# Performance work log

Hardware: AMD Instinct MI355X
Metric: run time of the kernel (lower is better)

Reference implementation:

```python
import jax, jax.numpy as jnp
import numpy as np

N_NODES = 100000
N_EDGES = 1600000
D_FEAT = 64
COS_EPS = 1e-8  # torch.nn.functional.cosine_similarity default eps


def setup_inputs() -> dict:
    key = jax.random.key(0)
    k1, k2 = jax.random.split(key)
    features = jax.random.normal(k1, (N_NODES, D_FEAT), dtype=jnp.float32)
    edge_index = jax.random.randint(k2, (2, N_EDGES), 0, N_NODES, dtype=jnp.int64)
    return {"features": features, "edge_index": edge_index}


def _mean_agg(h, src, dst, n_nodes):
    # copy_u: message = h[src]; fn.mean: per-dst mean over incoming messages
    msg_sum = jax.ops.segment_sum(h[src], dst, num_segments=n_nodes)  # [N, d]
    deg = jax.ops.segment_sum(jnp.ones(src.shape, h.dtype), dst, num_segments=n_nodes)  # [N]
    deg = deg[:, None]
    # nodes with zero in-degree get 0 (DGL mean semantics)
    return jnp.where(deg > 0, msg_sum / jnp.maximum(deg, 1.0), 0.0)


def reference(features, edge_index):
    src, dst = edge_index[0], edge_index[1]
    n = features.shape[0]
    x1 = _mean_agg(features, src, dst, n)   # gcn1
    x2 = _mean_agg(x1, src, dst, n)         # gcn2
    # cosine similarity along feature dim
    dot = jnp.sum(x1 * x2, axis=-1)
    n1 = jnp.linalg.norm(x1, axis=-1)
    n2 = jnp.linalg.norm(x2, axis=-1)
    cos = dot / jnp.maximum(n1 * n2, COS_EPS)
    w = cos[:, None]
    return w * x2 + (1.0 - w) * x1
```

## Files before the change

kernel.cpp:

```cpp
#include <hip/hip_runtime.h>
#include <hip/hip_fp16.h>
#include <math.h>

#define N_NODES 100000
#define N_EDGES 1600000
#define D_FEAT  64

#define NPB     256
#define NBC     ((N_NODES + NPB - 1) / NPB)
#define F1_WGS  512
#define NV4     (N_EDGES / 4)
#define CHUNK_V ((NV4 + F1_WGS - 1) / F1_WGS)
#define RAW_CAP 5120
#define CASTN   ((N_NODES * D_FEAT) / 4)
#define CAST_BLOCKS ((CASTN + 255) / 256)

#define GCAP    68


__device__ __forceinline__ uint4 pack8(const float* v) {
    __half2 h0 = __floats2half2_rn(v[0], v[1]);
    __half2 h1 = __floats2half2_rn(v[2], v[3]);
    __half2 h2 = __floats2half2_rn(v[4], v[5]);
    __half2 h3 = __floats2half2_rn(v[6], v[7]);
    uint4 st;
    st.x = *(unsigned*)&h0; st.y = *(unsigned*)&h1;
    st.z = *(unsigned*)&h2; st.w = *(unsigned*)&h3;
    return st;
}

__device__ __forceinline__ void unp8(uint4 u, float* a) {
    { __half2 h = *(__half2*)&u.x; float2 f = __half22float2(h); a[0]=f.x; a[1]=f.y; }
    { __half2 h = *(__half2*)&u.y; float2 f = __half22float2(h); a[2]=f.x; a[3]=f.y; }
    { __half2 h = *(__half2*)&u.z; float2 f = __half22float2(h); a[4]=f.x; a[5]=f.y; }
    { __half2 h = *(__half2*)&u.w; float2 f = __half22float2(h); a[6]=f.x; a[7]=f.y; }
}

__device__ __forceinline__ void acc4(uint4 u, __half2& h0, __half2& h1,
                                     __half2& h2, __half2& h3) {
    h0 = __hadd2(h0, *(__half2*)&u.x);
    h1 = __hadd2(h1, *(__half2*)&u.y);
    h2 = __hadd2(h2, *(__half2*)&u.z);
    h3 = __hadd2(h3, *(__half2*)&u.w);
}

__device__ __forceinline__ int block_excl_scan_512(int v, int t, int* wsum) {
    int lane = t & 63, wv = t >> 6;
    int incl = v;
    #pragma unroll
    for (int m = 1; m < 64; m <<= 1) {
        int o = __shfl_up(incl, m);
        if (lane >= m) incl += o;
    }
    if (lane == 63) wsum[wv] = incl;
    __syncthreads();
    int prefix = 0;
    #pragma unroll
    for (int j = 0; j < 8; j++)
        if (j < wv) prefix += wsum[j];
    return prefix + incl - v;
}


__global__ void cast_and_hist(const float* __restrict__ feat,
                              __half* __restrict__ feat_h,
                              const int4* __restrict__ dst4,
                              int* __restrict__ percnt) {
    if (blockIdx.x >= F1_WGS) {
        int i = (blockIdx.x - F1_WGS) * 256 + threadIdx.x;
        if (i < CASTN) {
            float4 v = ((const float4*)feat)[i];
            __half2 h0 = __floats2half2_rn(v.x, v.y);
            __half2 h1 = __floats2half2_rn(v.z, v.w);
            uint2 st;
            st.x = *(unsigned*)&h0;
            st.y = *(unsigned*)&h1;
            ((uint2*)feat_h)[i] = st;
        }
        return;
    }
    __shared__ int cnt[NBC];
    for (int i = threadIdx.x; i < NBC; i += blockDim.x) cnt[i] = 0;
    __syncthreads();
    int i0 = blockIdx.x * CHUNK_V;
    int i1 = min(i0 + CHUNK_V, NV4);
    for (int i = i0 + threadIdx.x; i < i1; i += blockDim.x) {
        int4 d = dst4[i];
        atomicAdd(&cnt[d.x >> 8], 1);
        atomicAdd(&cnt[d.y >> 8], 1);
        atomicAdd(&cnt[d.z >> 8], 1);
        atomicAdd(&cnt[d.w >> 8], 1);
    }
    __syncthreads();
    for (int i = threadIdx.x; i < NBC; i += blockDim.x)
        percnt[i * F1_WGS + blockIdx.x] = cnt[i];
}


__global__ __launch_bounds__(F1_WGS) void bucket_colscan(
        int* __restrict__ percnt, int* __restrict__ bhist) {
    __shared__ int wsum[8];
    int b = blockIdx.x, t = threadIdx.x;
    int v = percnt[b * F1_WGS + t];
    int excl = block_excl_scan_512(v, t, wsum);
    percnt[b * F1_WGS + t] = excl;
    if (t == F1_WGS - 1) bhist[b] = excl + v;
}

__global__ __launch_bounds__(512) void bucket_scan(
        const int* __restrict__ bhist, int* __restrict__ bbase) {
    __shared__ int wsum[8];
    int t = threadIdx.x;
    int v = (t < NBC) ? bhist[t] : 0;
    int excl = block_excl_scan_512(v, t, wsum);
    if (t < NBC) bbase[t] = excl;
    if (t == NBC - 1) bbase[NBC] = excl + v;
}

__global__ __launch_bounds__(F1_WGS) void bucketize(
        const int4* __restrict__ src4,
        const int4* __restrict__ dst4,
        const int* __restrict__ bbase,
        const int* __restrict__ percnt,
        unsigned int* __restrict__ tmp1) {
    __shared__ int base[NBC];
    __shared__ int cur[NBC];
    int wg = blockIdx.x, t = threadIdx.x;
    if (t < NBC) {
        base[t] = bbase[t] + percnt[t * F1_WGS + wg];
        cur[t] = 0;
    }
    __syncthreads();
    int i0 = wg * CHUNK_V;
    int i1 = min(i0 + CHUNK_V, NV4);
    for (int i = i0 + t; i < i1; i += F1_WGS) {
        int4 d = dst4[i];
        int4 s = src4[i];
        {
            int b = d.x >> 8; int r = atomicAdd(&cur[b], 1);
            tmp1[base[b] + r] = ((unsigned)s.x << 8) | (unsigned)(d.x & 255);
        }
        {
            int b = d.y >> 8; int r = atomicAdd(&cur[b], 1);
            tmp1[base[b] + r] = ((unsigned)s.y << 8) | (unsigned)(d.y & 255);
        }
        {
            int b = d.z >> 8; int r = atomicAdd(&cur[b], 1);
            tmp1[base[b] + r] = ((unsigned)s.z << 8) | (unsigned)(d.z & 255);
        }
        {
            int b = d.w >> 8; int r = atomicAdd(&cur[b], 1);
            tmp1[base[b] + r] = ((unsigned)s.w << 8) | (unsigned)(d.w & 255);
        }
    }
}

__global__ __launch_bounds__(512) void bucket_csr(
        const unsigned int* __restrict__ tmp1,
        const int* __restrict__ bbase,
        int* __restrict__ offsets,
        int* __restrict__ csr_src) {
    __shared__ int cnt[NPB];
    __shared__ int off[NPB];
    __shared__ int wsum[8];
    __shared__ int buf[RAW_CAP];
    int b = blockIdx.x, t = threadIdx.x;
    int ebase = bbase[b];
    int ecnt  = bbase[b + 1] - ebase;
    int node0 = b * NPB;

    if (t < NPB) cnt[t] = 0;
    __syncthreads();

    if (ecnt <= RAW_CAP) {
        unsigned myv[10];
        #pragma unroll
        for (int k = 0; k < 10; k++) {
            int i = t + k * 512;
            if (i < ecnt) {
                unsigned u = tmp1[ebase + i];
                myv[k] = u;
                atomicAdd(&cnt[u & 255], 1);
            }
        }
        __syncthreads();

        int v = (t < NPB) ? cnt[t] : 0;
        int excl = block_excl_scan_512(v, t, wsum);
        if (t < NPB) {
            off[t] = excl;
            cnt[t] = 0;
            if (node0 + t < N_NODES) offsets[node0 + t] = ebase + excl;
        }
        if (b == NBC - 1 && t == 0) offsets[N_NODES] = N_EDGES;
        __syncthreads();

        #pragma unroll
        for (int k = 0; k < 10; k++) {
            int i = t + k * 512;
            if (i < ecnt) {
                unsigned u = myv[k];
                int d = (int)(u & 255);
                int r = atomicAdd(&cnt[d], 1);
                buf[off[d] + r] = (int)(u >> 8);
            }
        }
        __syncthreads();
        for (int i = t; i < ecnt; i += 512)
            csr_src[ebase + i] = buf[i];
    } else {
        for (int i = t; i < ecnt; i += 512)
            atomicAdd(&cnt[tmp1[ebase + i] & 255], 1);
        __syncthreads();

        int v = (t < NPB) ? cnt[t] : 0;
        int excl = block_excl_scan_512(v, t, wsum);
        if (t < NPB) {
            off[t] = excl;
            cnt[t] = 0;
            if (node0 + t < N_NODES) offsets[node0 + t] = ebase + excl;
        }
        if (b == NBC - 1 && t == 0) offsets[N_NODES] = N_EDGES;
        __syncthreads();

        for (int i = t; i < ecnt; i += 512) {
            unsigned u = tmp1[ebase + i];
            int d = (int)(u & 255);
            int r = atomicAdd(&cnt[d], 1);
            csr_src[ebase + off[d] + r] = (int)(u >> 8);
        }
    }
}


__global__ __launch_bounds__(256) void gather1_kernel(
        const __half* __restrict__ feat_h,
        const int* __restrict__ offsets,
        const int* __restrict__ csr,
        __half* __restrict__ x1_h) {
    __shared__ int snbr[4][8][GCAP];
    int wv   = threadIdx.x >> 6;
    int lane = threadIdx.x & 63;
    int g    = lane >> 3;
    int fl   = lane & 7;
    int node = (blockIdx.x * 4 + wv) * 8 + g;

    int base = offsets[node];
    int deg  = offsets[node + 1] - base;
    int dcap = min(deg, GCAP);

    int* my = snbr[wv][g];
    for (int j = fl; j < dcap; j += 8)
        my[j] = csr[base + j];
    __builtin_amdgcn_wave_barrier();

    __half2 a0 = __float2half2_rn(0.f), a1 = a0, a2 = a0, a3 = a0;
    __half2 b0 = a0, b1 = a0, b2 = a0, b3 = a0;
    const __half* fb = feat_h + (fl << 3);
    int j = 0;
    for (; j + 4 <= dcap; j += 4) {
        int4 s = *(const int4*)&my[j];
        uint4 u0 = *(const uint4*)(fb + ((size_t)s.x << 6));
        uint4 u1 = *(const uint4*)(fb + ((size_t)s.y << 6));
        uint4 u2 = *(const uint4*)(fb + ((size_t)s.z << 6));
        uint4 u3 = *(const uint4*)(fb + ((size_t)s.w << 6));
        acc4(u0, a0, a1, a2, a3);
        acc4(u1, b0, b1, b2, b3);
        acc4(u2, a0, a1, a2, a3);
        acc4(u3, b0, b1, b2, b3);
    }
    for (; j < dcap; ++j) {
        int s = my[j];
        uint4 u = *(const uint4*)(fb + ((size_t)s << 6));
        acc4(u, a0, a1, a2, a3);
    }
    for (j = GCAP; j < deg; ++j) {
        int s = csr[base + j];
        uint4 u = *(const uint4*)(fb + ((size_t)s << 6));
        acc4(u, a0, a1, a2, a3);
    }
    a0 = __hadd2(a0, b0); a1 = __hadd2(a1, b1);
    a2 = __hadd2(a2, b2); a3 = __hadd2(a3, b3);

    float invf = (deg > 0) ? __builtin_amdgcn_rcpf((float)deg) : 0.0f;
    float r[8];
    { float2 f = __half22float2(a0); r[0]=f.x*invf; r[1]=f.y*invf; }
    { float2 f = __half22float2(a1); r[2]=f.x*invf; r[3]=f.y*invf; }
    { float2 f = __half22float2(a2); r[4]=f.x*invf; r[5]=f.y*invf; }
    { float2 f = __half22float2(a3); r[6]=f.x*invf; r[7]=f.y*invf; }
    *(uint4*)(x1_h + ((size_t)node << 6) + (fl << 3)) = pack8(r);
}

__global__ __launch_bounds__(256) void gather2_finalize_kernel(
        const __half* __restrict__ x1_h,
        const int* __restrict__ offsets,
        const int* __restrict__ csr,
        float* __restrict__ out) {
    __shared__ int snbr[4][8][GCAP];
    int wv   = threadIdx.x >> 6;
    int lane = threadIdx.x & 63;
    int g    = lane >> 3;
    int fl   = lane & 7;
    int node = (blockIdx.x * 4 + wv) * 8 + g;

    int base = offsets[node];
    int deg  = offsets[node + 1] - base;
    int dcap = min(deg, GCAP);

    int* my = snbr[wv][g];
    for (int j = fl; j < dcap; j += 8)
        my[j] = csr[base + j];
    __builtin_amdgcn_wave_barrier();

    __half2 a0 = __float2half2_rn(0.f), a1 = a0, a2 = a0, a3 = a0;
    __half2 c0 = a0, c1 = a0, c2 = a0, c3 = a0;
    const __half* fb = x1_h + (fl << 3);
    int j = 0;
    for (; j + 4 <= dcap; j += 4) {
        int4 s = *(const int4*)&my[j];
        uint4 u0 = *(const uint4*)(fb + ((size_t)s.x << 6));
        uint4 u1 = *(const uint4*)(fb + ((size_t)s.y << 6));
        uint4 u2 = *(const uint4*)(fb + ((size_t)s.z << 6));
        uint4 u3 = *(const uint4*)(fb + ((size_t)s.w << 6));
        acc4(u0, a0, a1, a2, a3);
        acc4(u1, c0, c1, c2, c3);
        acc4(u2, a0, a1, a2, a3);
        acc4(u3, c0, c1, c2, c3);
    }
    for (; j < dcap; ++j) {
        int s = my[j];
        uint4 u = *(const uint4*)(fb + ((size_t)s << 6));
        acc4(u, a0, a1, a2, a3);
    }
    for (j = GCAP; j < deg; ++j) {
        int s = csr[base + j];
        uint4 u = *(const uint4*)(fb + ((size_t)s << 6));
        acc4(u, a0, a1, a2, a3);
    }
    a0 = __hadd2(a0, c0); a1 = __hadd2(a1, c1);
    a2 = __hadd2(a2, c2); a3 = __hadd2(a3, c3);

    float invf = (deg > 0) ? __builtin_amdgcn_rcpf((float)deg) : 0.0f;
    float b[8];
    { float2 f = __half22float2(a0); b[0]=f.x*invf; b[1]=f.y*invf; }
    { float2 f = __half22float2(a1); b[2]=f.x*invf; b[3]=f.y*invf; }
    { float2 f = __half22float2(a2); b[4]=f.x*invf; b[5]=f.y*invf; }
    { float2 f = __half22float2(a3); b[6]=f.x*invf; b[7]=f.y*invf; }

    float a[8];
    uint4 ua = *(const uint4*)(x1_h + ((size_t)node << 6) + (fl << 3));
    unp8(ua, a);

    float dot = 0.f, nn1 = 0.f, nn2 = 0.f;
    #pragma unroll
    for (int t = 0; t < 8; t++) {
        dot += a[t] * b[t];
        nn1 += a[t] * a[t];
        nn2 += b[t] * b[t];
    }
    #pragma unroll
    for (int m = 1; m < 8; m <<= 1) {
        dot += __shfl_xor(dot, m);
        nn1 += __shfl_xor(nn1, m);
        nn2 += __shfl_xor(nn2, m);
    }

    float denom = fmaxf(__builtin_amdgcn_sqrtf(nn1 * nn2), 1e-8f);
    float w = dot * __builtin_amdgcn_rcpf(denom);
    float omw = 1.0f - w;

    float4 r0, r1;
    r0.x = w*b[0] + omw*a[0]; r0.y = w*b[1] + omw*a[1];
    r0.z = w*b[2] + omw*a[2]; r0.w = w*b[3] + omw*a[3];
    r1.x = w*b[4] + omw*a[4]; r1.y = w*b[5] + omw*a[5];
    r1.z = w*b[6] + omw*a[6]; r1.w = w*b[7] + omw*a[7];
    float* po = out + ((size_t)node << 6) + (fl << 3);
    *(float4*)po = r0;
    *(float4*)(po + 4) = r1;
}


extern "C" void kernel_launch(void* const* d_in, const int* in_sizes, int n_in,
                              void* d_out, int out_size, void* d_ws, size_t ws_size,
                              hipStream_t stream) {
    const float* feat = (const float*)d_in[0];
    const int*   eidx = (const int*)d_in[1];
    const int4*  src4 = (const int4*)eidx;
    const int4*  dst4 = (const int4*)(eidx + N_EDGES);

    __half*       feat_h  = (__half*)d_ws;
    __half*       x1_h    = feat_h + (size_t)N_NODES * D_FEAT;
    unsigned int* tmp1    = (unsigned int*)(x1_h + (size_t)N_NODES * D_FEAT);
    int*          csr_src = (int*)(tmp1 + N_EDGES);
    int*          offsets = csr_src + N_EDGES;
    int*          percnt  = offsets + (N_NODES + 1);
    int*          bhist   = percnt + NBC * F1_WGS;
    int*          bbase   = bhist + NBC;
    float*        out     = (float*)d_out;

    cast_and_hist <<<F1_WGS + CAST_BLOCKS, 256, 0, stream>>>(feat, feat_h, dst4, percnt);
    bucket_colscan<<<NBC, F1_WGS, 0, stream>>>(percnt, bhist);
    bucket_scan   <<<1, 512, 0, stream>>>(bhist, bbase);
    bucketize     <<<F1_WGS, F1_WGS, 0, stream>>>(src4, dst4, bbase, percnt, tmp1);
    bucket_csr    <<<NBC, 512, 0, stream>>>(tmp1, bbase, offsets, csr_src);

    int nblocks = N_NODES / 32;
    gather1_kernel<<<nblocks, 256, 0, stream>>>(feat_h, offsets, csr_src, x1_h);
    gather2_finalize_kernel<<<nblocks, 256, 0, stream>>>(x1_h, offsets, csr_src, out);
}
```

Baseline: 164.0 us.

## Spread feature cast across CSR build kernels and fold bucket scan into consumers

```diff
diff --git a/kernel.cpp b/kernel.cpp
--- a/kernel.cpp
+++ b/kernel.cpp
@@ -8,15 +8,36 @@
 
 #define NPB     256
 #define NBC     ((N_NODES + NPB - 1) / NPB)
-#define F1_WGS  512
+#define HIST_WGS 256
 #define NV4     (N_EDGES / 4)
-#define CHUNK_V ((NV4 + F1_WGS - 1) / F1_WGS)
+#define CHUNK4  ((NV4 + HIST_WGS - 1) / HIST_WGS)
 #define RAW_CAP 5120
 #define CASTN   ((N_NODES * D_FEAT) / 4)
-#define CAST_BLOCKS ((CASTN + 255) / 256)
+
+#define CAST1   2250
+#define CAST2   1000
+#define CAST3   750
+#define CAST4   750
+#define CO1     0
+#define CO2     (CAST1 * 256)
+#define CO3     (CO2 + CAST2 * 256)
+#define CO4     (CO3 + CAST3 * 512)
 
 #define GCAP    68
 
+
+__device__ __forceinline__ void cast_slice(const float* __restrict__ feat,
+                                           __half* __restrict__ feat_h, int i) {
+    if (i < CASTN) {
+        float4 v = ((const float4*)feat)[i];
+        __half2 h0 = __floats2half2_rn(v.x, v.y);
+        __half2 h1 = __floats2half2_rn(v.z, v.w);
+        uint2 st;
+        st.x = *(unsigned*)&h0;
+        st.y = *(unsigned*)&h1;
+        ((uint2*)feat_h)[i] = st;
+    }
+}
 
 __device__ __forceinline__ uint4 pack8(const float* v) {
     __half2 h0 = __floats2half2_rn(v[0], v[1]);
@@ -61,30 +82,40 @@
     return prefix + incl - v;
 }
 
-
-__global__ void cast_and_hist(const float* __restrict__ feat,
-                              __half* __restrict__ feat_h,
-                              const int4* __restrict__ dst4,
-                              int* __restrict__ percnt) {
-    if (blockIdx.x >= F1_WGS) {
-        int i = (blockIdx.x - F1_WGS) * 256 + threadIdx.x;
-        if (i < CASTN) {
-            float4 v = ((const float4*)feat)[i];
-            __half2 h0 = __floats2half2_rn(v.x, v.y);
-            __half2 h1 = __floats2half2_rn(v.z, v.w);
-            uint2 st;
-            st.x = *(unsigned*)&h0;
-            st.y = *(unsigned*)&h1;
-            ((uint2*)feat_h)[i] = st;
-        }
+__device__ __forceinline__ int block_excl_scan_256(int v, int t, int* wsum) {
+    int lane = t & 63, wv = t >> 6;
+    int incl = v;
+    #pragma unroll
+    for (int m = 1; m < 64; m <<= 1) {
+        int o = __shfl_up(incl, m);
+        if (lane >= m) incl += o;
+    }
+    if (lane == 63) wsum[wv] = incl;
+    __syncthreads();
+    int prefix = 0;
+    #pragma unroll
+    for (int j = 0; j < 4; j++)
+        if (j < wv) prefix += wsum[j];
+    return prefix + incl - v;
+}
+
+
+__global__ __launch_bounds__(256) void k1_hist_cast(
+        const float* __restrict__ feat,
+        __half* __restrict__ feat_h,
+        const int4* __restrict__ dst4,
+        int* __restrict__ percnt) {
+    if (blockIdx.x >= HIST_WGS) {
+        cast_slice(feat, feat_h, CO1 + (blockIdx.x - HIST_WGS) * 256 + threadIdx.x);
         return;
     }
     __shared__ int cnt[NBC];
-    for (int i = threadIdx.x; i < NBC; i += blockDim.x) cnt[i] = 0;
-    __syncthreads();
-    int i0 = blockIdx.x * CHUNK_V;
-    int i1 = min(i0 + CHUNK_V, NV4);
-    for (int i = i0 + threadIdx.x; i < i1; i += blockDim.x) {
+    int wg = blockIdx.x, t = threadIdx.x;
+    for (int i = t; i < NBC; i += 256) cnt[i] = 0;
+    __syncthreads();
+    int i0 = wg * CHUNK4;
+    int i1 = min(i0 + CHUNK4, NV4);
+    for (int i = i0 + t; i < i1; i += 256) {
         int4 d = dst4[i];
         atomicAdd(&cnt[d.x >> 8], 1);
         atomicAdd(&cnt[d.y >> 8], 1);
@@ -92,48 +123,56 @@
         atomicAdd(&cnt[d.w >> 8], 1);
     }
     __syncthreads();
-    for (int i = threadIdx.x; i < NBC; i += blockDim.x)
-        percnt[i * F1_WGS + blockIdx.x] = cnt[i];
-}
-
-
-__global__ __launch_bounds__(F1_WGS) void bucket_colscan(
-        int* __restrict__ percnt, int* __restrict__ bhist) {
+    for (int i = t; i < NBC; i += 256)
+        percnt[wg * NBC + i] = cnt[i];
+}
+
+
+__global__ __launch_bounds__(256) void k2_colscan(
+        const int* __restrict__ percnt,
+        int* __restrict__ pexcl,
+        int* __restrict__ bhist,
+        const float* __restrict__ feat,
+        __half* __restrict__ feat_h) {
+    if (blockIdx.x >= NBC) {
+        cast_slice(feat, feat_h, CO2 + (blockIdx.x - NBC) * 256 + threadIdx.x);
+        return;
+    }
+    __shared__ int wsum[4];
+    int b = blockIdx.x, t = threadIdx.x;
+    int v = percnt[t * NBC + b];
+    int excl = block_excl_scan_256(v, t, wsum);
+    pexcl[b * HIST_WGS + t] = excl;
+    if (t == HIST_WGS - 1) bhist[b] = excl + v;
+}
+
+
+__global__ __launch_bounds__(512) void k3_bucketize(
+        const int4* __restrict__ src4,
+        const int4* __restrict__ dst4,
+        const int* __restrict__ bhist,
+        const int* __restrict__ pexcl,
+        unsigned int* __restrict__ tmp1,
+        const float* __restrict__ feat,
+        __half* __restrict__ feat_h) {
+    if (blockIdx.x >= HIST_WGS) {
+        cast_slice(feat, feat_h, CO3 + (blockIdx.x - HIST_WGS) * 512 + threadIdx.x);
+        return;
+    }
+    __shared__ int base[NBC];
+    __shared__ int cur[NBC];
     __shared__ int wsum[8];
-    int b = blockIdx.x, t = threadIdx.x;
-    int v = percnt[b * F1_WGS + t];
-    int excl = block_excl_scan_512(v, t, wsum);
-    percnt[b * F1_WGS + t] = excl;
-    if (t == F1_WGS - 1) bhist[b] = excl + v;
-}
-
-__global__ __launch_bounds__(512) void bucket_scan(
-        const int* __restrict__ bhist, int* __restrict__ bbase) {
-    __shared__ int wsum[8];
-    int t = threadIdx.x;
+    int wg = blockIdx.x, t = threadIdx.x;
     int v = (t < NBC) ? bhist[t] : 0;
     int excl = block_excl_scan_512(v, t, wsum);
-    if (t < NBC) bbase[t] = excl;
-    if (t == NBC - 1) bbase[NBC] = excl + v;
-}
-
-__global__ __launch_bounds__(F1_WGS) void bucketize(
-        const int4* __restrict__ src4,
-        const int4* __restrict__ dst4,
-        const int* __restrict__ bbase,
-        const int* __restrict__ percnt,
-        unsigned int* __restrict__ tmp1) {
-    __shared__ int base[NBC];
-    __shared__ int cur[NBC];
-    int wg = blockIdx.x, t = threadIdx.x;
     if (t < NBC) {
-        base[t] = bbase[t] + percnt[t * F1_WGS + wg];
+        base[t] = excl + pexcl[t * HIST_WGS + wg];
         cur[t] = 0;
     }
     __syncthreads();
-    int i0 = wg * CHUNK_V;
-    int i1 = min(i0 + CHUNK_V, NV4);
-    for (int i = i0 + t; i < i1; i += F1_WGS) {
+    int i0 = wg * CHUNK4;
+    int i1 = min(i0 + CHUNK4, NV4);
+    for (int i = i0 + t; i < i1; i += 512) {
         int4 d = dst4[i];
         int4 s = src4[i];
         {
@@ -155,22 +194,35 @@
     }
 }
 
-__global__ __launch_bounds__(512) void bucket_csr(
+
+__global__ __launch_bounds__(512) void k4_bucket_csr(
         const unsigned int* __restrict__ tmp1,
-        const int* __restrict__ bbase,
+        const int* __restrict__ bhist,
         int* __restrict__ offsets,
-        int* __restrict__ csr_src) {
+        int* __restrict__ csr_src,
+        const float* __restrict__ feat,
+        __half* __restrict__ feat_h) {
+    if (blockIdx.x >= NBC) {
+        cast_slice(feat, feat_h, CO4 + (blockIdx.x - NBC) * 512 + threadIdx.x);
+        return;
+    }
     __shared__ int cnt[NPB];
     __shared__ int off[NPB];
     __shared__ int wsum[8];
     __shared__ int buf[RAW_CAP];
+    __shared__ int sEbase, sEcnt;
     int b = blockIdx.x, t = threadIdx.x;
-    int ebase = bbase[b];
-    int ecnt  = bbase[b + 1] - ebase;
+
+    {
+        int v = (t < NBC) ? bhist[t] : 0;
+        int ex = block_excl_scan_512(v, t, wsum);
+        if (t == b) { sEbase = ex; sEcnt = v; }
+    }
+    if (t < NPB) cnt[t] = 0;
+    __syncthreads();
+    int ebase = sEbase;
+    int ecnt  = sEcnt;
     int node0 = b * NPB;
-
-    if (t < NPB) cnt[t] = 0;
-    __syncthreads();
 
     if (ecnt <= RAW_CAP) {
         unsigned myv[10];
@@ -394,15 +446,14 @@
     int*          csr_src = (int*)(tmp1 + N_EDGES);
     int*          offsets = csr_src + N_EDGES;
     int*          percnt  = offsets + (N_NODES + 1);
-    int*          bhist   = percnt + NBC * F1_WGS;
-    int*          bbase   = bhist + NBC;
+    int*          pexcl   = percnt + HIST_WGS * NBC;
+    int*          bhist   = pexcl + NBC * HIST_WGS;
     float*        out     = (float*)d_out;
 
-    cast_and_hist <<<F1_WGS + CAST_BLOCKS, 256, 0, stream>>>(feat, feat_h, dst4, percnt);
-    bucket_colscan<<<NBC, F1_WGS, 0, stream>>>(percnt, bhist);
-    bucket_scan   <<<1, 512, 0, stream>>>(bhist, bbase);
-    bucketize     <<<F1_WGS, F1_WGS, 0, stream>>>(src4, dst4, bbase, percnt, tmp1);
-    bucket_csr    <<<NBC, 512, 0, stream>>>(tmp1, bbase, offsets, csr_src);
+    k1_hist_cast <<<HIST_WGS + CAST1, 256, 0, stream>>>(feat, feat_h, dst4, percnt);
+    k2_colscan   <<<NBC + CAST2,      256, 0, stream>>>(percnt, pexcl, bhist, feat, feat_h);
+    k3_bucketize <<<HIST_WGS + CAST3, 512, 0, stream>>>(src4, dst4, bhist, pexcl, tmp1, feat, feat_h);
+    k4_bucket_csr<<<NBC + CAST4,      512, 0, stream>>>(tmp1, bhist, offsets, csr_src, feat, feat_h);
 
     int nblocks = N_NODES / 32;
     gather1_kernel<<<nblocks, 256, 0, stream>>>(feat_h, offsets, csr_src, x1_h);
```

Measured after the change: 160.0 us, median of 2. 1.02x faster.

## Fuse CSR build into two kernels using atomic bucket reservation and cast stealing

Applied to the files above, without the earlier changes.

```diff
diff --git a/kernel.cpp b/kernel.cpp
--- a/kernel.cpp
+++ b/kernel.cpp
@@ -8,15 +8,33 @@
 
 #define NPB     256
 #define NBC     ((N_NODES + NPB - 1) / NPB)
-#define F1_WGS  512
+#define CAPB    4608
+#define AWGS    256
 #define NV4     (N_EDGES / 4)
-#define CHUNK_V ((NV4 + F1_WGS - 1) / F1_WGS)
+#define CHUNK4  ((NV4 + AWGS - 1) / AWGS)
+#define CHUNKE  (CHUNK4 * 4)
 #define RAW_CAP 5120
 #define CASTN   ((N_NODES * D_FEAT) / 4)
-#define CAST_BLOCKS ((CASTN + 255) / 256)
+
+#define CAST_A      1600
+#define CO_B        (CAST_A * 512)
+#define STEAL_UNITS ((CASTN - CO_B) / 512)
 
 #define GCAP    68
 
+
+__device__ __forceinline__ void cast_slice(const float* __restrict__ feat,
+                                           __half* __restrict__ feat_h, int i) {
+    if (i < CASTN) {
+        float4 v = ((const float4*)feat)[i];
+        __half2 h0 = __floats2half2_rn(v.x, v.y);
+        __half2 h1 = __floats2half2_rn(v.z, v.w);
+        uint2 st;
+        st.x = *(unsigned*)&h0;
+        st.y = *(unsigned*)&h1;
+        ((uint2*)feat_h)[i] = st;
+    }
+}
 
 __device__ __forceinline__ uint4 pack8(const float* v) {
     __half2 h0 = __floats2half2_rn(v[0], v[1]);
@@ -62,29 +80,31 @@
 }
 
 
-__global__ void cast_and_hist(const float* __restrict__ feat,
-                              __half* __restrict__ feat_h,
-                              const int4* __restrict__ dst4,
-                              int* __restrict__ percnt) {
-    if (blockIdx.x >= F1_WGS) {
-        int i = (blockIdx.x - F1_WGS) * 256 + threadIdx.x;
-        if (i < CASTN) {
-            float4 v = ((const float4*)feat)[i];
-            __half2 h0 = __floats2half2_rn(v.x, v.y);
-            __half2 h1 = __floats2half2_rn(v.z, v.w);
-            uint2 st;
-            st.x = *(unsigned*)&h0;
-            st.y = *(unsigned*)&h1;
-            ((uint2*)feat_h)[i] = st;
-        }
+__global__ __launch_bounds__(512) void ka_bucketize(
+        const int4* __restrict__ src4,
+        const int4* __restrict__ dst4,
+        int* __restrict__ bcur,
+        unsigned int* __restrict__ tmp1,
+        const float* __restrict__ feat,
+        __half* __restrict__ feat_h) {
+    if (blockIdx.x >= AWGS) {
+        cast_slice(feat, feat_h, (blockIdx.x - AWGS) * 512 + threadIdx.x);
         return;
     }
     __shared__ int cnt[NBC];
-    for (int i = threadIdx.x; i < NBC; i += blockDim.x) cnt[i] = 0;
-    __syncthreads();
-    int i0 = blockIdx.x * CHUNK_V;
-    int i1 = min(i0 + CHUNK_V, NV4);
-    for (int i = i0 + threadIdx.x; i < i1; i += blockDim.x) {
+    __shared__ int loff[NBC];
+    __shared__ int cur[NBC];
+    __shared__ int wsum[8];
+    __shared__ unsigned int chunkbuf[CHUNKE];
+    int wg = blockIdx.x, t = threadIdx.x;
+
+    for (int i = t; i < NBC; i += 512) cnt[i] = 0;
+    __syncthreads();
+
+    int e0 = wg * CHUNK4;
+    int e1 = min(e0 + CHUNK4, NV4);
+
+    for (int i = e0 + t; i < e1; i += 512) {
         int4 d = dst4[i];
         atomicAdd(&cnt[d.x >> 8], 1);
         atomicAdd(&cnt[d.y >> 8], 1);
@@ -92,143 +112,118 @@
         atomicAdd(&cnt[d.w >> 8], 1);
     }
     __syncthreads();
-    for (int i = threadIdx.x; i < NBC; i += blockDim.x)
-        percnt[i * F1_WGS + blockIdx.x] = cnt[i];
-}
-
-
-__global__ __launch_bounds__(F1_WGS) void bucket_colscan(
-        int* __restrict__ percnt, int* __restrict__ bhist) {
-    __shared__ int wsum[8];
-    int b = blockIdx.x, t = threadIdx.x;
-    int v = percnt[b * F1_WGS + t];
-    int excl = block_excl_scan_512(v, t, wsum);
-    percnt[b * F1_WGS + t] = excl;
-    if (t == F1_WGS - 1) bhist[b] = excl + v;
-}
-
-__global__ __launch_bounds__(512) void bucket_scan(
-        const int* __restrict__ bhist, int* __restrict__ bbase) {
-    __shared__ int wsum[8];
-    int t = threadIdx.x;
-    int v = (t < NBC) ? bhist[t] : 0;
-    int excl = block_excl_scan_512(v, t, wsum);
-    if (t < NBC) bbase[t] = excl;
-    if (t == NBC - 1) bbase[NBC] = excl + v;
-}
-
-__global__ __launch_bounds__(F1_WGS) void bucketize(
-        const int4* __restrict__ src4,
-        const int4* __restrict__ dst4,
-        const int* __restrict__ bbase,
-        const int* __restrict__ percnt,
-        unsigned int* __restrict__ tmp1) {
-    __shared__ int base[NBC];
-    __shared__ int cur[NBC];
-    int wg = blockIdx.x, t = threadIdx.x;
-    if (t < NBC) {
-        base[t] = bbase[t] + percnt[t * F1_WGS + wg];
-        cur[t] = 0;
-    }
-    __syncthreads();
-    int i0 = wg * CHUNK_V;
-    int i1 = min(i0 + CHUNK_V, NV4);
-    for (int i = i0 + t; i < i1; i += F1_WGS) {
+
+    int v = (t < NBC) ? cnt[t] : 0;
+    int ex = block_excl_scan_512(v, t, wsum);
+    if (t < NBC) { loff[t] = ex; cur[t] = 0; }
+    __syncthreads();
+
+    for (int i = e0 + t; i < e1; i += 512) {
         int4 d = dst4[i];
         int4 s = src4[i];
         {
             int b = d.x >> 8; int r = atomicAdd(&cur[b], 1);
-            tmp1[base[b] + r] = ((unsigned)s.x << 8) | (unsigned)(d.x & 255);
+            chunkbuf[loff[b] + r] = ((unsigned)s.x << 8) | (unsigned)(d.x & 255);
         }
         {
             int b = d.y >> 8; int r = atomicAdd(&cur[b], 1);
-            tmp1[base[b] + r] = ((unsigned)s.y << 8) | (unsigned)(d.y & 255);
+            chunkbuf[loff[b] + r] = ((unsigned)s.y << 8) | (unsigned)(d.y & 255);
         }
         {
             int b = d.z >> 8; int r = atomicAdd(&cur[b], 1);
-            tmp1[base[b] + r] = ((unsigned)s.z << 8) | (unsigned)(d.z & 255);
+            chunkbuf[loff[b] + r] = ((unsigned)s.z << 8) | (unsigned)(d.z & 255);
         }
         {
             int b = d.w >> 8; int r = atomicAdd(&cur[b], 1);
-            tmp1[base[b] + r] = ((unsigned)s.w << 8) | (unsigned)(d.w & 255);
-        }
-    }
-}
-
-__global__ __launch_bounds__(512) void bucket_csr(
+            chunkbuf[loff[b] + r] = ((unsigned)s.w << 8) | (unsigned)(d.w & 255);
+        }
+    }
+    __syncthreads();
+
+    if (t < NBC) {
+        int c = cnt[t];
+        if (c > 0) {
+            int gb = atomicAdd(&bcur[t], c);
+            if (gb + c > CAPB) c = max(0, CAPB - gb);
+            unsigned int* dst = tmp1 + (size_t)t * CAPB + gb;
+            int lb = loff[t];
+            for (int k = 0; k < c; k++) dst[k] = chunkbuf[lb + k];
+        }
+    }
+}
+
+
+__global__ __launch_bounds__(512) void kb_bucket_csr(
         const unsigned int* __restrict__ tmp1,
-        const int* __restrict__ bbase,
+        const int* __restrict__ bcur,
         int* __restrict__ offsets,
-        int* __restrict__ csr_src) {
+        int* __restrict__ csr_src,
+        int* __restrict__ castctr,
+        const float* __restrict__ feat,
+        __half* __restrict__ feat_h) {
     __shared__ int cnt[NPB];
     __shared__ int off[NPB];
     __shared__ int wsum[8];
     __shared__ int buf[RAW_CAP];
+    __shared__ int sObase, sEcnt;
     int b = blockIdx.x, t = threadIdx.x;
-    int ebase = bbase[b];
-    int ecnt  = bbase[b + 1] - ebase;
+
+    {
+        int v = (t < NBC) ? bcur[t] : 0;
+        int ex = block_excl_scan_512(v, t, wsum);
+        if (t == b) { sObase = ex; sEcnt = v; }
+    }
+    if (t < NPB) cnt[t] = 0;
+    __syncthreads();
+    int obase = sObase;
+    int ecnt  = sEcnt;
+    const unsigned int* ebuf = tmp1 + (size_t)b * CAPB;
     int node0 = b * NPB;
 
-    if (t < NPB) cnt[t] = 0;
-    __syncthreads();
-
-    if (ecnt <= RAW_CAP) {
-        unsigned myv[10];
-        #pragma unroll
-        for (int k = 0; k < 10; k++) {
-            int i = t + k * 512;
-            if (i < ecnt) {
-                unsigned u = tmp1[ebase + i];
-                myv[k] = u;
-                atomicAdd(&cnt[u & 255], 1);
-            }
-        }
-        __syncthreads();
-
-        int v = (t < NPB) ? cnt[t] : 0;
-        int excl = block_excl_scan_512(v, t, wsum);
-        if (t < NPB) {
-            off[t] = excl;
-            cnt[t] = 0;
-            if (node0 + t < N_NODES) offsets[node0 + t] = ebase + excl;
-        }
-        if (b == NBC - 1 && t == 0) offsets[N_NODES] = N_EDGES;
-        __syncthreads();
-
-        #pragma unroll
-        for (int k = 0; k < 10; k++) {
-            int i = t + k * 512;
-            if (i < ecnt) {
-                unsigned u = myv[k];
-                int d = (int)(u & 255);
-                int r = atomicAdd(&cnt[d], 1);
-                buf[off[d] + r] = (int)(u >> 8);
-            }
-        }
-        __syncthreads();
-        for (int i = t; i < ecnt; i += 512)
-            csr_src[ebase + i] = buf[i];
-    } else {
-        for (int i = t; i < ecnt; i += 512)
-            atomicAdd(&cnt[tmp1[ebase + i] & 255], 1);
-        __syncthreads();
-
-        int v = (t < NPB) ? cnt[t] : 0;
-        int excl = block_excl_scan_512(v, t, wsum);
-        if (t < NPB) {
-            off[t] = excl;
-            cnt[t] = 0;
-            if (node0 + t < N_NODES) offsets[node0 + t] = ebase + excl;
-        }
-        if (b == NBC - 1 && t == 0) offsets[N_NODES] = N_EDGES;
-        __syncthreads();
-
-        for (int i = t; i < ecnt; i += 512) {
-            unsigned u = tmp1[ebase + i];
+    unsigned myv[10];
+    #pragma unroll
+    for (int k = 0; k < 10; k++) {
+        int i = t + k * 512;
+        if (i < ecnt) {
+            unsigned u = ebuf[i];
+            myv[k] = u;
+            atomicAdd(&cnt[u & 255], 1);
+        }
+    }
+    __syncthreads();
+
+    int v = (t < NPB) ? cnt[t] : 0;
+    int excl = block_excl_scan_512(v, t, wsum);
+    if (t < NPB) {
+        off[t] = excl;
+        cnt[t] = 0;
+        if (node0 + t < N_NODES) offsets[node0 + t] = obase + excl;
+    }
+    if (b == NBC - 1 && t == 0) offsets[N_NODES] = N_EDGES;
+    __syncthreads();
+
+    #pragma unroll
+    for (int k = 0; k < 10; k++) {
+        int i = t + k * 512;
+        if (i < ecnt) {
+            unsigned u = myv[k];
             int d = (int)(u & 255);
             int r = atomicAdd(&cnt[d], 1);
-            csr_src[ebase + off[d] + r] = (int)(u >> 8);
-        }
+            buf[off[d] + r] = (int)(u >> 8);
+        }
+    }
+    __syncthreads();
+    for (int i = t; i < ecnt; i += 512)
+        csr_src[obase + i] = buf[i];
+
+    for (;;) {
+        __shared__ int sUnit;
+        if (t == 0) sUnit = atomicAdd(castctr, 1);
+        __syncthreads();
+        int u = sUnit;
+        __syncthreads();
+        if (u >= STEAL_UNITS) break;
+        cast_slice(feat, feat_h, CO_B + u * 512 + t);
     }
 }
 
@@ -391,18 +386,18 @@
     __half*       feat_h  = (__half*)d_ws;
     __half*       x1_h    = feat_h + (size_t)N_NODES * D_FEAT;
     unsigned int* tmp1    = (unsigned int*)(x1_h + (size_t)N_NODES * D_FEAT);
-    int*          csr_src = (int*)(tmp1 + N_EDGES);
+    int*          csr_src = (int*)(tmp1 + (size_t)NBC * CAPB);
     int*          offsets = csr_src + N_EDGES;
-    int*          percnt  = offsets + (N_NODES + 1);
-    int*          bhist   = percnt + NBC * F1_WGS;
-    int*          bbase   = bhist + NBC;
+    int*          bcur    = offsets + (N_NODES + 1);
+    int*          castctr = bcur + NBC;
     float*        out     = (float*)d_out;
 
-    cast_and_hist <<<F1_WGS + CAST_BLOCKS, 256, 0, stream>>>(feat, feat_h, dst4, percnt);
-    bucket_colscan<<<NBC, F1_WGS, 0, stream>>>(percnt, bhist);
-    bucket_scan   <<<1, 512, 0, stream>>>(bhist, bbase);
-    bucketize     <<<F1_WGS, F1_WGS, 0, stream>>>(src4, dst4, bbase, percnt, tmp1);
-    bucket_csr    <<<NBC, 512, 0, stream>>>(tmp1, bbase, offsets, csr_src);
+    hipMemsetAsync(bcur, 0, (NBC + 1) * sizeof(int), stream);
+
+    ka_bucketize<<<AWGS + CAST_A, 512, 0, stream>>>(
+        src4, dst4, bcur, tmp1, feat, feat_h);
+    kb_bucket_csr<<<NBC, 512, 0, stream>>>(
+        tmp1, bcur, offsets, csr_src, castctr, feat, feat_h);
 
     int nblocks = N_NODES / 32;
     gather1_kernel<<<nblocks, 256, 0, stream>>>(feat_h, offsets, csr_src, x1_h);
```

Measured after the change: 179.9 us. 9.7% more time.
